# Optimization experiments

Hardware: AMD Instinct MI355X
Metric: run time of the kernel (lower is better)

Reference implementation:

```python
import jax, jax.numpy as jnp
import numpy as np

DIM = 64
K = 8
B_TAIL = 3.0
HID = 128
BATCH = 131072
MIN_BIN_WIDTH = 1e-3
MIN_BIN_HEIGHT = 1e-3
MIN_DERIVATIVE = 1e-3


def setup_inputs() -> dict:
    key = jax.random.key(0)
    ks = jax.random.split(key, 9)
    nin = DIM // 2
    nout = (3 * K - 1) * (DIM - DIM // 2)
    dims = [nin, HID, HID, HID, nout]
    d = {"x": jax.random.normal(ks[0], (BATCH, DIM), jnp.float32)}
    for i in range(4):
        d[f"W{i+1}"] = jax.random.normal(ks[1 + 2 * i], (dims[i], dims[i + 1]), jnp.float32) / jnp.sqrt(dims[i])
        d[f"b{i+1}"] = jax.random.normal(ks[2 + 2 * i], (dims[i + 1],), jnp.float32) * 0.01
    return d


def _gather(a, idx):
    # a: [..., K or K+1], idx: [...] int -> [...]
    return jnp.take_along_axis(a, idx[..., None], axis=-1)[..., 0]


def _mlp(x, W1, b1, W2, b2, W3, b3, W4, b4):
    h = jax.nn.elu(x @ W1 + b1)
    h = jax.nn.elu(h @ W2 + b2)
    h = jax.nn.elu(h @ W3 + b3)
    return h @ W4 + b4


def _unconstrained_rqs_fwd(inputs, uw, uh, ud, tail_bound):
    # inputs: [B, D2]; uw/uh: [B, D2, K]; ud: [B, D2, K-1]
    num_bins = uw.shape[-1]
    left = bottom = -tail_bound
    right = top = tail_bound

    inside = (inputs >= -tail_bound) & (inputs <= tail_bound)
    x = jnp.clip(inputs, -tail_bound, tail_bound)  # safe values for spline math

    # pad derivatives and pin boundary slopes so spline matches identity tails
    const = float(np.log(np.exp(1.0 - MIN_DERIVATIVE) - 1.0))
    ud = jnp.pad(ud, [(0, 0)] * (ud.ndim - 1) + [(1, 1)], constant_values=const)

    widths = jax.nn.softmax(uw, axis=-1)
    widths = MIN_BIN_WIDTH + (1.0 - MIN_BIN_WIDTH * num_bins) * widths
    cumwidths = jnp.cumsum(widths, axis=-1)
    cumwidths = jnp.pad(cumwidths, [(0, 0)] * (cumwidths.ndim - 1) + [(1, 0)])
    cumwidths = (right - left) * cumwidths + left
    cumwidths = cumwidths.at[..., 0].set(left).at[..., -1].set(right)
    widths = cumwidths[..., 1:] - cumwidths[..., :-1]

    derivatives = MIN_DERIVATIVE + jax.nn.softplus(ud)

    heights = jax.nn.softmax(uh, axis=-1)
    heights = MIN_BIN_HEIGHT + (1.0 - MIN_BIN_HEIGHT * num_bins) * heights
    cumheights = jnp.cumsum(heights, axis=-1)
    cumheights = jnp.pad(cumheights, [(0, 0)] * (cumheights.ndim - 1) + [(1, 0)])
    cumheights = (top - bottom) * cumheights + bottom
    cumheights = cumheights.at[..., 0].set(bottom).at[..., -1].set(top)
    heights = cumheights[..., 1:] - cumheights[..., :-1]

    # searchsorted: number of bin edges <= x, minus one (eps on last edge)
    cw = cumwidths.at[..., -1].add(1e-6)
    bin_idx = jnp.sum((x[..., None] >= cw).astype(jnp.int32), axis=-1) - 1
    bin_idx = jnp.clip(bin_idx, 0, num_bins - 1)

    in_cw = _gather(cumwidths, bin_idx)
    in_w = _gather(widths, bin_idx)
    in_ch = _gather(cumheights, bin_idx)
    in_h = _gather(heights, bin_idx)
    delta = heights / widths
    in_delta = _gather(delta, bin_idx)
    in_d = _gather(derivatives, bin_idx)
    in_d1 = _gather(derivatives[..., 1:], bin_idx)

    theta = (x - in_cw) / in_w
    t1mt = theta * (1.0 - theta)
    numerator = in_h * (in_delta * theta ** 2 + in_d * t1mt)
    denominator = in_delta + (in_d + in_d1 - 2.0 * in_delta) * t1mt
    spline_out = in_ch + numerator / denominator
    deriv_num = in_delta ** 2 * (in_d1 * theta ** 2 + 2.0 * in_delta * t1mt + in_d * (1.0 - theta) ** 2)
    spline_ld = jnp.log(deriv_num) - 2.0 * jnp.log(denominator)

    outputs = jnp.where(inside, spline_out, inputs)
    logabsdet = jnp.where(inside, spline_ld, 0.0)
    return outputs, logabsdet


def reference(x, W1, b1, W2, b2, W3, b3, W4, b4):
    d_half = DIM // 2
    x1, x2 = x[:, :d_half], x[:, d_half:]
    out = _mlp(x1, W1, b1, W2, b2, W3, b3, W4, b4)
    out = out.reshape(-1, DIM - d_half, 3 * K - 1)
    W = out[..., :K]
    H = out[..., K:2 * K]
    D = out[..., 2 * K:]
    y2, ld = _unconstrained_rqs_fwd(x2, W, H, D, B_TAIL)
    log_det = jnp.sum(ld, axis=1)
    return jnp.concatenate([x1, y2], axis=1), log_det
```

## Files before the change

kernel.cpp:

```cpp
#include <hip/hip_runtime.h>
#include <hip/hip_bf16.h>
#include <math.h>

typedef _Float16 f16_t;
typedef _Float16 f16x4 __attribute__((ext_vector_type(4)));
typedef _Float16 f16x8 __attribute__((ext_vector_type(8)));
typedef float f32x4 __attribute__((ext_vector_type(4)));

#define BATCH 131072
#define MTILE 64
#define NBLK (BATCH / MTILE)

#define W1F 0
#define W2F 4096
#define W3F 20480
#define W4F 36864

__global__ __launch_bounds__(256) void convert_weights_kernel(
    const float* __restrict__ W1, const float* __restrict__ W2,
    const float* __restrict__ W3, const float* __restrict__ W4,
    f16_t* __restrict__ wf) {
  int tid = blockIdx.x * 256 + threadIdx.x;
  if (tid >= 16896) return;
  int lane = tid & 63;
  int l16 = lane & 15, lhi = lane >> 4;
  const float* W; int ncols, col, k0; bool zero = false;
  if (tid < 512) {
    int n = tid >> 6;
    W = W1; ncols = 128; col = n * 16 + l16; k0 = lhi * 8;
  } else if (tid < 2560) {
    int g = tid - 512; int n = g >> 8, s = (g >> 6) & 3;
    W = W2; ncols = 128; col = n * 16 + l16; k0 = s * 32 + lhi * 8;
  } else if (tid < 4608) {
    int g = tid - 2560; int n = g >> 8, s = (g >> 6) & 3;
    W = W3; ncols = 128; col = n * 16 + l16; k0 = s * 32 + lhi * 8;
  } else {
    int g = tid - 4608; int t = g >> 8, s = (g >> 6) & 3;
    int c = t / 6, n = t - c * 6;
    int colc = n * 16 + l16;
    W = W4; ncols = 736; col = c * 92 + colc; k0 = s * 32 + lhi * 8;
    zero = (colc >= 92);
  }
  f16x8 v;
#pragma unroll
  for (int j = 0; j < 8; ++j)
    v[j] = zero ? (f16_t)0.f : (f16_t)W[(k0 + j) * ncols + col];
  *(f16x8*)(wf + (size_t)tid * 8) = v;
}

__device__ __forceinline__ float elu(float v) {
  return v > 0.f ? v : (__expf(v) - 1.f);
}

__device__ __forceinline__ void rqs_task(const f16_t* P, float xv,
                                         float& yout, float& ldout) {
  f16x8 pw = *(const f16x8*)P;
  f16x8 ph = *(const f16x8*)(P + 8);
  f16x8 pd = *(const f16x8*)(P + 16);

  float ew[8], sw = 0.f;
#pragma unroll
  for (int i = 0; i < 8; ++i) { ew[i] = __expf((float)pw[i]); sw += ew[i]; }
  float invw = 0.992f * __builtin_amdgcn_rcpf(sw);
  float cw[9]; cw[0] = -3.f;
  float accw = 0.f;
#pragma unroll
  for (int i = 0; i < 8; ++i) {
    accw += 0.001f + ew[i] * invw;
    cw[i + 1] = -3.f + 6.f * accw;
  }
  cw[8] = 3.f;
  float wd[8];
#pragma unroll
  for (int i = 0; i < 8; ++i) wd[i] = cw[i + 1] - cw[i];

  float eh[8], sh = 0.f;
#pragma unroll
  for (int i = 0; i < 8; ++i) { eh[i] = __expf((float)ph[i]); sh += eh[i]; }
  float invh = 0.992f * __builtin_amdgcn_rcpf(sh);
  float ch[9]; ch[0] = -3.f;
  float acch = 0.f;
#pragma unroll
  for (int i = 0; i < 8; ++i) {
    acch += 0.001f + eh[i] * invh;
    ch[i + 1] = -3.f + 6.f * acch;
  }
  ch[8] = 3.f;
  float ht[8];
#pragma unroll
  for (int i = 0; i < 8; ++i) ht[i] = ch[i + 1] - ch[i];

  float dd[9]; dd[0] = 1.f; dd[8] = 1.f;
#pragma unroll
  for (int i = 0; i < 7; ++i) {
    float u = (float)pd[i];
    float sp = fmaxf(u, 0.f) + __logf(1.f + __expf(-fabsf(u)));
    dd[i + 1] = 0.001f + sp;
  }

  float xc = fminf(fmaxf(xv, -3.f), 3.f);
  int bin = 0;
#pragma unroll
  for (int i = 1; i < 8; ++i) bin += (xc >= cw[i]) ? 1 : 0;

  float in_cw = cw[0], in_w = wd[0], in_ch = ch[0], in_h = ht[0];
  float in_d = dd[0], in_d1 = dd[1];
#pragma unroll
  for (int i = 1; i < 8; ++i) {
    bool g = (bin >= i);
    in_cw = g ? cw[i] : in_cw;  in_w = g ? wd[i] : in_w;
    in_ch = g ? ch[i] : in_ch;  in_h = g ? ht[i] : in_h;
    in_d  = g ? dd[i] : in_d;   in_d1 = g ? dd[i + 1] : in_d1;
  }

  float rw = __builtin_amdgcn_rcpf(in_w);
  float dlt = in_h * rw;
  float th = (xc - in_cw) * rw;
  float om = 1.f - th;
  float t1 = th * om;
  float num = in_h * (dlt * th * th + in_d * t1);
  float den = dlt + (in_d + in_d1 - 2.f * dlt) * t1;
  float rden = __builtin_amdgcn_rcpf(den);
  float yo = in_ch + num * rden;
  float dn = dlt * dlt * (in_d1 * th * th + 2.f * dlt * t1 + in_d * om * om);
  float ldv = __logf(dn * rden * rden);
  bool inside = (xv >= -3.f) && (xv <= 3.f);
  yout = inside ? yo : xv;
  ldout = inside ? ldv : 0.f;
}

__device__ __forceinline__ void mid_layer_ip(f16_t* hH,
                                             const f16_t* __restrict__ wseg,
                                             const float* __restrict__ bg,
                                             int wv, int l16, int lhi, int lane) {
  f16x8 a[4];
#pragma unroll
  for (int s = 0; s < 4; ++s)
    a[s] = *(const f16x8*)&hH[(wv * 16 + l16) * 136 + s * 32 + lhi * 8];
#pragma unroll
  for (int n = 0; n < 8; ++n) {
    f32x4 acc = {0.f, 0.f, 0.f, 0.f};
#pragma unroll
    for (int s = 0; s < 4; ++s) {
      f16x8 b = *(const f16x8*)(wseg + (size_t)((n * 4 + s) * 64 + lane) * 8);
      acc = __builtin_amdgcn_mfma_f32_16x16x32_f16(a[s], b, acc, 0, 0, 0);
    }
    float bias = bg[n * 16 + l16];
#pragma unroll
    for (int r = 0; r < 4; ++r)
      hH[(wv * 16 + lhi * 4 + r) * 136 + n * 16 + l16] =
          (f16_t)elu(acc[r] + bias);
  }
}

__global__ __launch_bounds__(256, 4) void nsf_fused_kernel(
    const float* __restrict__ x,
    const float* __restrict__ b1g, const float* __restrict__ b2g,
    const float* __restrict__ b3g, const float* __restrict__ b4g,
    const f16_t* __restrict__ wf,
    float* __restrict__ out) {
  __shared__ f16_t hH[MTILE * 136];
  __shared__ f16_t prm[MTILE * 4 * 24];
  __shared__ float x2s[MTILE * 33];

  const int tid = threadIdx.x;
  const int lane = tid & 63;
  const int wv = tid >> 6;
  const int l16 = lane & 15, lhi = lane >> 4;
  const int row0 = blockIdx.x * MTILE;

  {
    const float4* x4 = (const float4*)(x + (size_t)row0 * 64);
    float4* o4 = (float4*)(out + (size_t)row0 * 64);
#pragma unroll
    for (int it = 0; it < 4; ++it) {
      int idx = tid + it * 256;
      int row = idx >> 4, q = idx & 15;
      float4 v = x4[row * 16 + q];
      if (q < 8) {
        o4[row * 16 + q] = v;
        f16x4 p = {(f16_t)v.x, (f16_t)v.y, (f16_t)v.z, (f16_t)v.w};
        *(f16x4*)&hH[row * 136 + q * 4] = p;
      } else {
        int cb = row * 33 + (q - 8) * 4;
        x2s[cb + 0] = v.x; x2s[cb + 1] = v.y;
        x2s[cb + 2] = v.z; x2s[cb + 3] = v.w;
      }
    }
  }
  __syncthreads();

  {
    f16x8 a = *(const f16x8*)&hH[(wv * 16 + l16) * 136 + lhi * 8];
#pragma unroll
    for (int n = 0; n < 8; ++n) {
      f16x8 b = *(const f16x8*)(wf + W1F + (size_t)(n * 64 + lane) * 8);
      f32x4 acc = {0.f, 0.f, 0.f, 0.f};
      acc = __builtin_amdgcn_mfma_f32_16x16x32_f16(a, b, acc, 0, 0, 0);
      float bias = b1g[n * 16 + l16];
#pragma unroll
      for (int r = 0; r < 4; ++r)
        hH[(wv * 16 + lhi * 4 + r) * 136 + n * 16 + l16] =
            (f16_t)elu(acc[r] + bias);
    }
  }
  __syncthreads();

  mid_layer_ip(hH, wf + W2F, b2g, wv, l16, lhi, lane);
  __syncthreads();
  mid_layer_ip(hH, wf + W3F, b3g, wv, l16, lhi, lane);
  __syncthreads();

  {
    f16x8 a4[4];
#pragma unroll
    for (int s = 0; s < 4; ++s)
      a4[s] = *(const f16x8*)&hH[(wv * 16 + l16) * 136 + s * 32 + lhi * 8];

    const int srow = tid >> 2;
    const int sjj = tid & 3;
    float ldp = 0.f;

    for (int c = 0; c < 8; ++c) {
#pragma unroll
      for (int n = 0; n < 6; ++n) {
        f32x4 acc = {0.f, 0.f, 0.f, 0.f};
#pragma unroll
        for (int s = 0; s < 4; ++s) {
          f16x8 b = *(const f16x8*)(wf + W4F +
                      (size_t)(((c * 6 + n) * 4 + s) * 64 + lane) * 8);
          acc = __builtin_amdgcn_mfma_f32_16x16x32_f16(a4[s], b, acc, 0, 0, 0);
        }
        int colc = n * 16 + l16;
        if (colc < 92) {
          int dm = (colc * 90) >> 11;
          int j = colc - dm * 23;
          float bias = b4g[c * 92 + colc];
#pragma unroll
          for (int r = 0; r < 4; ++r)
            prm[((wv * 16 + lhi * 4 + r) * 4 + dm) * 24 + j] =
                (f16_t)(acc[r] + bias);
        }
      }
      __syncthreads();

      {
        int jg = c * 4 + sjj;
        float xv = x2s[srow * 33 + jg];
        float y0, l0;
        rqs_task(prm + (srow * 4 + sjj) * 24, xv, y0, l0);
        out[(size_t)(row0 + srow) * 64 + 32 + jg] = y0;
        ldp += l0;
      }
      __syncthreads();
    }

    ldp += __shfl_xor(ldp, 1, 64);
    ldp += __shfl_xor(ldp, 2, 64);
    if ((tid & 3) == 0)
      out[(size_t)BATCH * 64 + row0 + srow] = ldp;
  }
}

extern "C" void kernel_launch(void* const* d_in, const int* in_sizes, int n_in,
                              void* d_out, int out_size, void* d_ws, size_t ws_size,
                              hipStream_t stream) {
  const float* x  = (const float*)d_in[0];
  const float* W1 = (const float*)d_in[1];
  const float* b1 = (const float*)d_in[2];
  const float* W2 = (const float*)d_in[3];
  const float* b2 = (const float*)d_in[4];
  const float* W3 = (const float*)d_in[5];
  const float* b3 = (const float*)d_in[6];
  const float* W4 = (const float*)d_in[7];
  const float* b4 = (const float*)d_in[8];
  f16_t* wf = (f16_t*)d_ws;
  float* out = (float*)d_out;

  hipLaunchKernelGGL(convert_weights_kernel, dim3(66), dim3(256), 0, stream,
                     W1, W2, W3, W4, wf);
  hipLaunchKernelGGL(nsf_fused_kernel, dim3(NBLK), dim3(256), 0, stream,
                     x, b1, b2, b3, b4, wf, out);
}
```

Before: 107.1 us.

## Swizzle LDS, use per-wave barriers, compute softplus only for selected bins

Each wave now works only on its own 16 rows. This allows the two block-wide barriers in the layer-4 and spline loop to become wave barriers. The hidden-activation LDS buffer drops its padding and uses an XOR swizzle to avoid bank conflicts. The x2 tail is stored as fp16 to shrink LDS, and launch bounds are raised to 5 blocks per CU. The spline now evaluates softplus only for the two derivatives of the selected bin instead of all seven. Storing x2 in fp16 loses precision on the pass-through outputs and spline inputs, which is a correctness risk.

```diff
diff --git a/kernel.cpp b/kernel.cpp
--- a/kernel.cpp
+++ b/kernel.cpp
@@ -15,6 +15,10 @@
 #define W2F 4096
 #define W3F 20480
 #define W4F 36864
+
+__device__ __forceinline__ int hsw(int r, int e) {
+  return r * 128 + (e ^ ((r & 7) << 3));
+}
 
 __global__ __launch_bounds__(256) void convert_weights_kernel(
     const float* __restrict__ W1, const float* __restrict__ W2,
@@ -90,28 +94,29 @@
 #pragma unroll
   for (int i = 0; i < 8; ++i) ht[i] = ch[i + 1] - ch[i];
 
-  float dd[9]; dd[0] = 1.f; dd[8] = 1.f;
-#pragma unroll
-  for (int i = 0; i < 7; ++i) {
-    float u = (float)pd[i];
-    float sp = fmaxf(u, 0.f) + __logf(1.f + __expf(-fabsf(u)));
-    dd[i + 1] = 0.001f + sp;
-  }
-
   float xc = fminf(fmaxf(xv, -3.f), 3.f);
   int bin = 0;
 #pragma unroll
   for (int i = 1; i < 8; ++i) bin += (xc >= cw[i]) ? 1 : 0;
 
   float in_cw = cw[0], in_w = wd[0], in_ch = ch[0], in_h = ht[0];
-  float in_d = dd[0], in_d1 = dd[1];
+  float sd  = (float)pd[0];
+  float sd1 = (float)pd[0];
 #pragma unroll
   for (int i = 1; i < 8; ++i) {
     bool g = (bin >= i);
     in_cw = g ? cw[i] : in_cw;  in_w = g ? wd[i] : in_w;
     in_ch = g ? ch[i] : in_ch;  in_h = g ? ht[i] : in_h;
-    in_d  = g ? dd[i] : in_d;   in_d1 = g ? dd[i + 1] : in_d1;
-  }
+    sd    = g ? (float)pd[i - 1] : sd;
+  }
+#pragma unroll
+  for (int i = 1; i < 7; ++i)
+    sd1 = (bin >= i) ? (float)pd[i] : sd1;
+
+  float spd  = fmaxf(sd,  0.f) + __logf(1.f + __expf(-fabsf(sd)));
+  float spd1 = fmaxf(sd1, 0.f) + __logf(1.f + __expf(-fabsf(sd1)));
+  float in_d  = (bin == 0) ? 1.f : 0.001f + spd;
+  float in_d1 = (bin == 7) ? 1.f : 0.001f + spd1;
 
   float rw = __builtin_amdgcn_rcpf(in_w);
   float dlt = in_h * rw;
@@ -129,14 +134,14 @@
   ldout = inside ? ldv : 0.f;
 }
 
-__device__ __forceinline__ void mid_layer_ip(f16_t* hH,
+__device__ __forceinline__ void mid_layer_ip(f16_t* hW,
                                              const f16_t* __restrict__ wseg,
                                              const float* __restrict__ bg,
-                                             int wv, int l16, int lhi, int lane) {
+                                             int l16, int lhi, int lane) {
   f16x8 a[4];
 #pragma unroll
   for (int s = 0; s < 4; ++s)
-    a[s] = *(const f16x8*)&hH[(wv * 16 + l16) * 136 + s * 32 + lhi * 8];
+    a[s] = *(const f16x8*)&hW[hsw(l16, s * 32 + lhi * 8)];
 #pragma unroll
   for (int n = 0; n < 8; ++n) {
     f32x4 acc = {0.f, 0.f, 0.f, 0.f};
@@ -148,26 +153,26 @@
     float bias = bg[n * 16 + l16];
 #pragma unroll
     for (int r = 0; r < 4; ++r)
-      hH[(wv * 16 + lhi * 4 + r) * 136 + n * 16 + l16] =
-          (f16_t)elu(acc[r] + bias);
-  }
-}
-
-__global__ __launch_bounds__(256, 4) void nsf_fused_kernel(
+      hW[hsw(lhi * 4 + r, n * 16 + l16)] = (f16_t)elu(acc[r] + bias);
+  }
+}
+
+__global__ __launch_bounds__(256, 5) void nsf_fused_kernel(
     const float* __restrict__ x,
     const float* __restrict__ b1g, const float* __restrict__ b2g,
     const float* __restrict__ b3g, const float* __restrict__ b4g,
     const f16_t* __restrict__ wf,
     float* __restrict__ out) {
-  __shared__ f16_t hH[MTILE * 136];
+  __shared__ f16_t hH[MTILE * 128];
   __shared__ f16_t prm[MTILE * 4 * 24];
-  __shared__ float x2s[MTILE * 33];
+  __shared__ f16_t x2s[MTILE * 32];
 
   const int tid = threadIdx.x;
   const int lane = tid & 63;
   const int wv = tid >> 6;
   const int l16 = lane & 15, lhi = lane >> 4;
   const int row0 = blockIdx.x * MTILE;
+  f16_t* hW = hH + wv * 16 * 128;
 
   {
     const float4* x4 = (const float4*)(x + (size_t)row0 * 64);
@@ -177,21 +182,19 @@
       int idx = tid + it * 256;
       int row = idx >> 4, q = idx & 15;
       float4 v = x4[row * 16 + q];
+      f16x4 p = {(f16_t)v.x, (f16_t)v.y, (f16_t)v.z, (f16_t)v.w};
       if (q < 8) {
         o4[row * 16 + q] = v;
-        f16x4 p = {(f16_t)v.x, (f16_t)v.y, (f16_t)v.z, (f16_t)v.w};
-        *(f16x4*)&hH[row * 136 + q * 4] = p;
+        *(f16x4*)&hH[hsw(row, q * 4)] = p;
       } else {
-        int cb = row * 33 + (q - 8) * 4;
-        x2s[cb + 0] = v.x; x2s[cb + 1] = v.y;
-        x2s[cb + 2] = v.z; x2s[cb + 3] = v.w;
+        *(f16x4*)&x2s[row * 32 + (q - 8) * 4] = p;
       }
     }
   }
   __syncthreads();
 
   {
-    f16x8 a = *(const f16x8*)&hH[(wv * 16 + l16) * 136 + lhi * 8];
+    f16x8 a = *(const f16x8*)&hW[hsw(l16, lhi * 8)];
 #pragma unroll
     for (int n = 0; n < 8; ++n) {
       f16x8 b = *(const f16x8*)(wf + W1F + (size_t)(n * 64 + lane) * 8);
@@ -200,22 +203,21 @@
       float bias = b1g[n * 16 + l16];
 #pragma unroll
       for (int r = 0; r < 4; ++r)
-        hH[(wv * 16 + lhi * 4 + r) * 136 + n * 16 + l16] =
-            (f16_t)elu(acc[r] + bias);
-    }
-  }
-  __syncthreads();
-
-  mid_layer_ip(hH, wf + W2F, b2g, wv, l16, lhi, lane);
-  __syncthreads();
-  mid_layer_ip(hH, wf + W3F, b3g, wv, l16, lhi, lane);
+        hW[hsw(lhi * 4 + r, n * 16 + l16)] = (f16_t)elu(acc[r] + bias);
+    }
+  }
+  __syncthreads();
+
+  mid_layer_ip(hW, wf + W2F, b2g, l16, lhi, lane);
+  __syncthreads();
+  mid_layer_ip(hW, wf + W3F, b3g, l16, lhi, lane);
   __syncthreads();
 
   {
     f16x8 a4[4];
 #pragma unroll
     for (int s = 0; s < 4; ++s)
-      a4[s] = *(const f16x8*)&hH[(wv * 16 + l16) * 136 + s * 32 + lhi * 8];
+      a4[s] = *(const f16x8*)&hW[hsw(l16, s * 32 + lhi * 8)];
 
     const int srow = tid >> 2;
     const int sjj = tid & 3;
@@ -242,17 +244,17 @@
                 (f16_t)(acc[r] + bias);
         }
       }
-      __syncthreads();
+      __builtin_amdgcn_wave_barrier();
 
       {
         int jg = c * 4 + sjj;
-        float xv = x2s[srow * 33 + jg];
+        float xv = (float)x2s[srow * 32 + jg];
         float y0, l0;
-        rqs_task(prm + (srow * 4 + sjj) * 24, xv, y0, l0);
+        rqs_task(prm + tid * 24, xv, y0, l0);
         out[(size_t)(row0 + srow) * 64 + 32 + jg] = y0;
         ldp += l0;
       }
-      __syncthreads();
+      __builtin_amdgcn_wave_barrier();
     }
 
     ldp += __shfl_xor(ldp, 1, 64);
```

Result: slower. 140.4 us (+31.2%).
